# Optimization experiments

Measured on AMD Instinct MI355X. Metric: run time of the kernel, lower is better.

The kernel has to match this reference:

```python
import jax, jax.numpy as jnp
import numpy as np

B, T, A, K, STEPS, E = 2, 16384, 128, 128, 16, 126


def soft_dirac_last(x):
    # softmax forward-replaced by one-hot(argmax), straight-through backward
    sm = jax.nn.softmax(x, axis=-1)
    hard = jax.nn.one_hot(jnp.argmax(x, axis=-1), x.shape[-1], dtype=x.dtype)
    return sm + jax.lax.stop_gradient(hard - sm)


def _encode(x, d_unit, atom_embeddings):
    # x: (B,1,T); d_unit: (A,K) unit-norm atoms
    rng = jnp.linspace(0.0, 1.0, T, dtype=x.dtype)
    kernel = d_unit[:, None, :]  # OIH
    pad = [(K // 2, K - 1 - K // 2)]  # SAME
    batch_ix = jnp.arange(B)

    def step(res, _):
        # dense feature map: correlation of residual with every atom
        fm = jax.lax.conv_general_dilated(
            res, kernel, window_strides=(1,), padding=pad,
            dimension_numbers=("NCH", "OIH", "NCH"))  # (B,A,T)
        flat = fm.reshape(B, A * T)
        fi = jnp.argmax(flat, axis=-1)                      # sparsify n_to_keep=1
        value = jnp.take_along_axis(flat, fi[:, None], axis=-1)  # (B,1)
        ai = fi // T
        ti = fi % T
        # position: soft_dirac over time of sparse fm summed over atoms
        pos_row = jnp.zeros((B, T), x.dtype).at[batch_ix, ti].set(value[:, 0])
        pd = soft_dirac_last(pos_row)
        position = jnp.sum(pd * rng[None, :], axis=-1, keepdims=True) * 20.0  # (B,1)
        # atom one-hot: soft_dirac over atom axis of sparse fm summed over time
        atom_row = jnp.zeros((B, A), x.dtype).at[batch_ix, ai].set(value[:, 0])
        ad = soft_dirac_last(atom_row)
        ae = ad @ atom_embeddings  # (B,E)
        emb = jnp.concatenate([position, value, ae], axis=-1)  # (B, 2+E)
        # matching-pursuit residual update: subtract value * atom at found shift
        recon = value * d_unit[ai]  # (B,K)
        buf = jnp.zeros((B, T + K), x.dtype)
        buf = jax.vmap(lambda bb, rr, tt: jax.lax.dynamic_update_slice(bb, rr, (tt,)))(buf, recon, ti)
        res = res - buf[:, None, K // 2:K // 2 + T]
        return res, emb

    res, embs = jax.lax.scan(step, x, None, length=STEPS)
    embs = jnp.transpose(embs, (1, 0, 2))  # (B, STEPS, 2+E)
    return embs, res


def _canonical_ordering(embs, proj):
    keys = embs @ proj  # (B, STEPS)
    order = jnp.argsort(keys, axis=-1)
    return jnp.take_along_axis(embs, order[:, :, None], axis=1)


def setup_inputs() -> dict:
    key = jax.random.key(0)
    ks = jax.random.split(key, 5)
    return {
        "a": jax.random.normal(ks[0], (B, 1, T), jnp.float32),
        "b": jax.random.normal(ks[1], (B, 1, T), jnp.float32),
        "d": jax.random.normal(ks[2], (A, K), jnp.float32),
        "atom_embeddings": jax.random.normal(ks[3], (A, E), jnp.float32) * 0.1,
        "ordering_proj": jax.random.normal(ks[4], (128,), jnp.float32),
    }


def reference(a, b, d, atom_embeddings, ordering_proj):
    d_unit = d / (jnp.linalg.norm(d, axis=-1, keepdims=True) + 1e-8)
    ae, a_res = _encode(a, d_unit, atom_embeddings)
    be, b_res = _encode(b, d_unit, atom_embeddings)
    ae = _canonical_ordering(ae, ordering_proj)
    be = _canonical_ordering(be, ordering_proj)
    a_norm = jnp.linalg.norm(a_res.reshape(-1, T), axis=-1)
    b_norm = jnp.linalg.norm(b_res.reshape(-1, T), axis=-1)
    return jnp.mean((ae - be) ** 2) + jnp.mean(jnp.abs(a_norm - b_norm))
```

## Files before the change

kernel.cpp:

```cpp
#include <hip/hip_runtime.h>
#include <math.h>

#define T_DIM 16384
#define A_DIM 128
#define K_DIM 128
#define N_STEPS 16
#define E_DIM 126
#define NSEQ 4

#define ATI 16
#define TT 256
#define NPT 512
#define NCB 32
#define HB 8192
#define RL_LEN 8319
#define RL_PAD 8608
#define SS_LEN 383
#define SS_PAD 404

#define PIDX(i) ((i) + ((i) >> 5))

__device__ inline unsigned long long pack_vi(float v, int fi) {
    unsigned int b = __float_as_uint(v);
    b = (b & 0x80000000u) ? ~b : (b | 0x80000000u);
    return ((unsigned long long)b << 32) | (unsigned int)(~fi);
}
__device__ inline void unpack_vi(unsigned long long p, float* v, int* fi) {
    unsigned int lo = (unsigned int)(p & 0xffffffffu);
    unsigned int b = (unsigned int)(p >> 32);
    unsigned int fb = (b & 0x80000000u) ? (b & 0x7fffffffu) : ~b;
    *v = __uint_as_float(fb);
    *fi = (int)(~lo);
}

__device__ inline unsigned long long u64max(unsigned long long a, unsigned long long b) {
    return a > b ? a : b;
}

__global__ __launch_bounds__(256) void k_prep(
    const float* __restrict__ d, const float* __restrict__ a,
    const float* __restrict__ b, float* __restrict__ du,
    float* __restrict__ res, int* __restrict__ cnt,
    unsigned long long* __restrict__ slots) {
    int blk = blockIdx.x, tid = threadIdx.x;
    if (blk < 128) {
        __shared__ float s[128];
        float v = 0.0f;
        if (tid < 128) { v = d[blk * K_DIM + tid]; s[tid] = v * v; }
        __syncthreads();
        for (int off = 64; off > 0; off >>= 1) {
            if (tid < off) s[tid] += s[tid + off];
            __syncthreads();
        }
        if (tid < 128) du[blk * K_DIM + tid] = v / (sqrtf(s[0]) + 1e-8f);
    } else if (blk < 384) {
        int i = (blk - 128) * 256 + tid;
        res[i] = (i < 2 * T_DIM) ? a[i] : b[i - 2 * T_DIM];
    } else {
        if (tid < NSEQ) cnt[tid] = 0;
        for (int i = tid; i < (N_STEPS - 1) * NSEQ * 16 + (N_STEPS - 1) * NSEQ;
             i += 256) slots[i] = 0ULL;
    }
}

__device__ inline unsigned long long tile_compute(
    const float* __restrict__ duP, const float* __restrict__ rsh,
    int L0, int a_lo, int t_lo, int tid, unsigned long long* red4) {

    float acc[4][4];
    #pragma unroll
    for (int i = 0; i < 4; i++)
        #pragma unroll
        for (int j = 0; j < 4; j++) acc[i][j] = 0.0f;

    float r[8];
    #pragma unroll
    for (int m = 0; m < 8; m++) r[m] = rsh[PIDX(L0 + m)];

    #pragma unroll 4
    for (int k = 0; k < K_DIM; k += 4) {
        float dA[4][4];
        #pragma unroll
        for (int i = 0; i < 4; i++)
            *(float4*)dA[i] = *(const float4*)(duP + i * K_DIM + k);
        #pragma unroll
        for (int dk = 0; dk < 4; dk++) {
            #pragma unroll
            for (int i = 0; i < 4; i++) {
                float s = dA[i][dk];
                #pragma unroll
                for (int j = 0; j < 4; j++)
                    acc[i][j] = fmaf(s, r[j + dk], acc[i][j]);
            }
        }
        r[0] = r[4]; r[1] = r[5]; r[2] = r[6]; r[3] = r[7];
        #pragma unroll
        for (int m = 0; m < 4; m++) r[4 + m] = rsh[PIDX(L0 + k + 8 + m)];
    }

    float bv = -INFINITY;
    int bi = 0x7fffffff;
    #pragma unroll
    for (int i = 0; i < 4; i++) {
        int a = a_lo + i;
        #pragma unroll
        for (int j = 0; j < 4; j++) {
            int fi = a * T_DIM + t_lo + j;
            float v = acc[i][j];
            if (v > bv || (v == bv && fi < bi)) { bv = v; bi = fi; }
        }
    }
    #pragma unroll
    for (int off = 32; off > 0; off >>= 1) {
        float v2 = __shfl_down(bv, off);
        int   i2 = __shfl_down(bi, off);
        if (v2 > bv || (v2 == bv && i2 < bi)) { bv = v2; bi = i2; }
    }
    if ((tid & 63) == 0) red4[tid >> 6] = pack_vi(bv, bi);
    __syncthreads();
    if (tid == 0) {
        unsigned long long m = red4[0];
        #pragma unroll
        for (int w = 1; w < 4; w++) if (red4[w] > m) m = red4[w];
        red4[0] = m;
    }
    __syncthreads();
    return red4[0];
}

__global__ __launch_bounds__(256) void k_step_full(
    float* __restrict__ res, const float* __restrict__ du,
    const float* __restrict__ ae, float* __restrict__ emb,
    unsigned long long* __restrict__ pmax, int* __restrict__ cnt,
    int* __restrict__ dirty0) {

    int seq = blockIdx.y;
    int blk = blockIdx.x;
    int a_base = (blk >> 6) * ATI;
    int t0 = (blk & 63) * TT;
    int tid = threadIdx.x;

    __shared__ float rsh[SS_PAD];
    __shared__ unsigned long long red4[4];
    __shared__ unsigned long long pm_sh[256];
    __shared__ int last_flag;

    const float* resS = res + seq * T_DIM;
    for (int i = tid; i < SS_LEN; i += 256) {
        int t = t0 - 64 + i;
        rsh[PIDX(i)] = (t >= 0 && t < T_DIM) ? resS[t] : 0.0f;
    }
    __syncthreads();

    int tg = tid & 63;
    int ag = __builtin_amdgcn_readfirstlane(tid >> 6);
    unsigned long long p = tile_compute(du + (a_base + ag * 4) * K_DIM, rsh,
                                        4 * tg, a_base + ag * 4, t0 + 4 * tg,
                                        tid, red4);
    if (tid == 0) {
        pmax[seq * NPT + blk] = p;
        __threadfence();
        last_flag = (atomicAdd(&cnt[seq], 1) == NPT - 1);
    }
    __syncthreads();
    if (!last_flag) return;

    __threadfence();
    {
        unsigned long long m0 = pmax[seq * NPT + tid];
        unsigned long long m1 = pmax[seq * NPT + 256 + tid];
        pm_sh[tid] = u64max(m0, m1);
    }
    __syncthreads();
    for (int off = 128; off > 0; off >>= 1) {
        if (tid < off) pm_sh[tid] = u64max(pm_sh[tid], pm_sh[tid + off]);
        __syncthreads();
    }
    float value; int fi;
    unpack_vi(pm_sh[0], &value, &fi);
    int ai = fi >> 14;
    int ti = fi & (T_DIM - 1);
    int pos_idx = value > 0.0f ? ti : 0;
    int atom_idx = value > 0.0f ? ai : 0;

    float* e = emb + (seq * N_STEPS + 0) * 128;
    if (tid == 0) {
        e[0] = ((float)pos_idx / (float)(T_DIM - 1)) * 20.0f;
        e[1] = value;
        int nlo = ti - (K_DIM - 1); if (nlo < 0) nlo = 0;
        int nhi = ti + K_DIM;       if (nhi > T_DIM) nhi = T_DIM;
        dirty0[seq * 2 + 0] = nlo;
        dirty0[seq * 2 + 1] = nhi;
    }
    if (tid >= 2 && tid < 2 + E_DIM) e[tid] = ae[atom_idx * E_DIM + tid - 2];
    if (tid >= 128) {
        int k = tid - 128;
        int t = ti + k - K_DIM / 2;
        if (t >= 0 && t < T_DIM) {
            float r = res[seq * T_DIM + t];
            res[seq * T_DIM + t] = __fsub_rn(r, __fmul_rn(value, du[ai * K_DIM + k]));
        }
    }
}

__global__ __launch_bounds__(256) void k_inc(
    float* __restrict__ res, const float* __restrict__ du,
    const float* __restrict__ ae, float* __restrict__ emb,
    const unsigned long long* __restrict__ pmax,
    unsigned long long* __restrict__ dslots,
    unsigned long long* __restrict__ wslots, const int* __restrict__ dirty0) {

    int seq = blockIdx.y;
    int blk = blockIdx.x;
    int tid = threadIdx.x;

    if (blk == NCB) {
        __shared__ unsigned long long table[NPT];
        __shared__ unsigned long long red4[4];
        __shared__ unsigned long long wsh;
        for (int i = tid; i < NPT; i += 256) table[i] = pmax[seq * NPT + i];
        int lo = dirty0[seq * 2 + 0];
        int hi = dirty0[seq * 2 + 1];
        __syncthreads();

        for (int step = 1; step < N_STEPS; step++) {
            int T0 = lo >> 8, T1 = T0 + 1;
            bool hasT1 = (T1 < 64) && (T1 * TT < hi);
            if (tid < 16) {
                int a = tid >> 1, w = tid & 1;
                if (w == 0 || hasT1) {
                    const unsigned long long* sp =
                        &dslots[((step - 1) * NSEQ + seq) * 16 + tid];
                    unsigned long long v = __hip_atomic_load(sp, __ATOMIC_RELAXED,
                                                             __HIP_MEMORY_SCOPE_AGENT);
                    while (v == 0ULL) {
                        __builtin_amdgcn_s_sleep(1);
                        v = __hip_atomic_load(sp, __ATOMIC_RELAXED,
                                              __HIP_MEMORY_SCOPE_AGENT);
                    }
                    table[a * 64 + (w ? T1 : T0)] = v;
                }
            }
            __syncthreads();
            unsigned long long m = u64max(table[tid], table[tid + 256]);
            #pragma unroll
            for (int off = 32; off > 0; off >>= 1)
                m = u64max(m, __shfl_down(m, off));
            if ((tid & 63) == 0) red4[tid >> 6] = m;
            __syncthreads();
            if (tid == 0) {
                unsigned long long w = red4[0];
                #pragma unroll
                for (int j = 1; j < 4; j++) w = u64max(w, red4[j]);
                wsh = w;
                atomicExch(&wslots[(step - 1) * NSEQ + seq], w);
            }
            __syncthreads();
            float value; int fi;
            unpack_vi(wsh, &value, &fi);
            int ti = fi & (T_DIM - 1);
            int ai = fi >> 14;
            int pos_idx = value > 0.0f ? ti : 0;
            int atom_idx = value > 0.0f ? ai : 0;
            float* e = emb + (seq * N_STEPS + step) * 128;
            if (tid == 0) {
                e[0] = ((float)pos_idx / (float)(T_DIM - 1)) * 20.0f;
                e[1] = value;
            }
            if (tid >= 2 && tid < 128) e[tid] = ae[atom_idx * E_DIM + tid - 2];
            lo = ti - (K_DIM - 1); if (lo < 0) lo = 0;
            hi = ti + K_DIM;       if (hi > T_DIM) hi = T_DIM;
        }
        return;
    }

    int atile = blk >> 2;
    int half = (blk >> 1) & 1;
    int par = blk & 1;
    int a_base = atile * ATI;
    int base = half * HB;

    __shared__ float resL[RL_PAD];
    __shared__ unsigned long long red4[4];
    __shared__ unsigned long long wsh;

    const float* resG = res + seq * T_DIM;
    for (int i4 = tid * 4; i4 < RL_LEN; i4 += 1024) {
        int t = base - 64 + i4;
        if (t >= 0 && t + 3 < T_DIM && i4 + 3 < RL_LEN) {
            float4 v = *(const float4*)&resG[t];
            resL[PIDX(i4 + 0)] = v.x; resL[PIDX(i4 + 1)] = v.y;
            resL[PIDX(i4 + 2)] = v.z; resL[PIDX(i4 + 3)] = v.w;
        } else {
            for (int m = 0; m < 4 && i4 + m < RL_LEN; m++) {
                int t2 = t + m;
                resL[PIDX(i4 + m)] = (t2 >= 0 && t2 < T_DIM) ? resG[t2] : 0.0f;
            }
        }
    }
    int lo = dirty0[seq * 2 + 0];
    int hi = dirty0[seq * 2 + 1];
    __syncthreads();

    for (int step = 1; step < N_STEPS; step++) {
        int T0 = lo >> 8, T1 = T0 + 1;
        int cand = -1;
        if (((T0 & 1) == par) && ((T0 >> 5) == half)) cand = T0;
        else if (T1 < 64 && ((T1 & 1) == par) && ((T1 >> 5) == half) &&
                 T1 * TT < hi) cand = T1;

        if (cand >= 0) {
            int t0 = cand * TT;
            int tg = tid & 63;
            int ag = __builtin_amdgcn_readfirstlane(tid >> 6);
            unsigned long long p = tile_compute(
                du + (a_base + ag * 4) * K_DIM, resL,
                (t0 - base) + 4 * tg, a_base + ag * 4, t0 + 4 * tg, tid, red4);
            if (tid == 0)
                atomicExch(&dslots[((step - 1) * NSEQ + seq) * 16 +
                                   atile * 2 + (cand == T1 ? 1 : 0)], p);
        }
        if (tid == 0) {
            const unsigned long long* sp = &wslots[(step - 1) * NSEQ + seq];
            unsigned long long v = __hip_atomic_load(sp, __ATOMIC_RELAXED,
                                                     __HIP_MEMORY_SCOPE_AGENT);
            while (v == 0ULL) {
                __builtin_amdgcn_s_sleep(2);
                v = __hip_atomic_load(sp, __ATOMIC_RELAXED,
                                      __HIP_MEMORY_SCOPE_AGENT);
            }
            wsh = v;
        }
        __syncthreads();
        float value; int fi;
        unpack_vi(wsh, &value, &fi);
        int ti = fi & (T_DIM - 1);
        int ai = fi >> 14;
        if (tid < 128) {
            int t = ti - K_DIM / 2 + tid;
            if (t >= 0 && t < T_DIM) {
                int L = t - base + 64;
                if (L >= 0 && L < RL_LEN) {
                    float r = resL[PIDX(L)];
                    resL[PIDX(L)] = __fsub_rn(r, __fmul_rn(value, du[ai * K_DIM + tid]));
                }
            }
        }
        __syncthreads();
        lo = ti - (K_DIM - 1); if (lo < 0) lo = 0;
        hi = ti + K_DIM;       if (hi > T_DIM) hi = T_DIM;
    }

    if (atile == 0 && par == 0) {
        float* resW = res + seq * T_DIM + base;
        for (int t = tid; t < HB; t += 256) resW[t] = resL[PIDX(t + 64)];
    }
}

__global__ __launch_bounds__(1024) void k_tail(
    const float* __restrict__ res, const float* __restrict__ emb,
    const float* __restrict__ proj, float* __restrict__ out) {
    int tid = threadIdx.x;
    __shared__ float sh[1024];
    __shared__ float norms[NSEQ];
    __shared__ float keys[NSEQ][N_STEPS];
    __shared__ int   order[NSEQ][N_STEPS];

    {
        int seq = tid >> 8;
        int ln  = tid & 255;
        const float4* r4 = (const float4*)(res + seq * T_DIM);
        float s = 0.0f;
        #pragma unroll
        for (int j = 0; j < 16; j++) {
            float4 v = r4[j * 256 + ln];
            s = fmaf(v.x, v.x, s); s = fmaf(v.y, v.y, s);
            s = fmaf(v.z, v.z, s); s = fmaf(v.w, v.w, s);
        }
        sh[tid] = s;
        __syncthreads();
        for (int off = 128; off > 0; off >>= 1) {
            if (ln < off) sh[tid] += sh[tid + off];
            __syncthreads();
        }
        if (ln == 0) norms[seq] = sqrtf(sh[tid]);
        __syncthreads();
    }
    {
        int pair = tid >> 4;
        int seq = pair >> 4, st = pair & 15;
        int ln = tid & 15;
        const float* e = emb + (seq * N_STEPS + st) * 128 + ln * 8;
        const float* pr = proj + ln * 8;
        float kk = 0.0f;
        #pragma unroll
        for (int dd = 0; dd < 8; dd++) kk = fmaf(e[dd], pr[dd], kk);
        sh[tid] = kk;
        __syncthreads();
        for (int off = 8; off > 0; off >>= 1) {
            if (ln < off) sh[tid] += sh[tid + off];
            __syncthreads();
        }
        if (ln == 0) keys[seq][st] = sh[tid];
        __syncthreads();
    }
    if (tid < NSEQ) {
        int ord[N_STEPS];
        for (int i = 0; i < N_STEPS; i++) ord[i] = i;
        for (int i = 1; i < N_STEPS; i++) {
            int oi = ord[i];
            float kv = keys[tid][oi];
            int j = i - 1;
            while (j >= 0 && keys[tid][ord[j]] > kv) { ord[j + 1] = ord[j]; j--; }
            ord[j + 1] = oi;
        }
        for (int i = 0; i < N_STEPS; i++) order[tid][i] = ord[i];
    }
    __syncthreads();
    float s = 0.0f;
    #pragma unroll
    for (int t = 0; t < 4; t++) {
        int idx = tid + t * 1024;
        int b  = idx >> 11;
        int st = (idx >> 7) & 15;
        int dd = idx & 127;
        float va = emb[((b    ) * N_STEPS + order[b    ][st]) * 128 + dd];
        float vb = emb[((2 + b) * N_STEPS + order[2 + b][st]) * 128 + dd];
        float df = va - vb;
        s = fmaf(df, df, s);
    }
    sh[tid] = s;
    __syncthreads();
    for (int off = 512; off > 0; off >>= 1) {
        if (tid < off) sh[tid] += sh[tid + off];
        __syncthreads();
    }
    if (tid == 0) {
        float mse = sh[0] / 4096.0f;
        float mad = 0.5f * (fabsf(norms[0] - norms[2]) + fabsf(norms[1] - norms[3]));
        out[0] = mse + mad;
    }
}

extern "C" void kernel_launch(void* const* d_in, const int* in_sizes, int n_in,
                              void* d_out, int out_size, void* d_ws, size_t ws_size,
                              hipStream_t stream) {
    const float* a    = (const float*)d_in[0];
    const float* b    = (const float*)d_in[1];
    const float* d    = (const float*)d_in[2];
    const float* ae   = (const float*)d_in[3];
    const float* proj = (const float*)d_in[4];
    float* out = (float*)d_out;

    float* ws  = (float*)d_ws;
    float* res = ws;
    float* du  = res + NSEQ * T_DIM;
    float* emb = du + A_DIM * K_DIM;
    unsigned long long* pmax   = (unsigned long long*)(emb + NSEQ * N_STEPS * 128);
    unsigned long long* dslots = pmax + NSEQ * NPT;
    unsigned long long* wslots = dslots + (N_STEPS - 1) * NSEQ * 16;
    int* cnt    = (int*)(wslots + (N_STEPS - 1) * NSEQ);
    int* dirty0 = cnt + NSEQ;

    k_prep<<<385, 256, 0, stream>>>(d, a, b, du, res, cnt, dslots);

    dim3 gfull(NPT, NSEQ);
    k_step_full<<<gfull, 256, 0, stream>>>(res, du, ae, emb, pmax, cnt, dirty0);

    dim3 ginc(NCB + 1, NSEQ);
    k_inc<<<ginc, 256, 0, stream>>>(res, du, ae, emb, pmax, dslots, wslots, dirty0);

    k_tail<<<1, 1024, 0, stream>>>(res, emb, proj, out);
}
```

Baseline: 235.1 us.

## Drop global residual buffer, halve atom tile, fold norm into incremental kernel

The separate residual copy is removed: the full-step and incremental kernels read the inputs a/b directly, and the first matching-pursuit subtraction is applied on the fly while loading into shared memory. The atom tile is halved from 16 to 8 atoms per block, which doubles the number of tiles in the full pass and in the incremental pass. That gives more parallelism, but each tile does less reuse. Residual norms are now accumulated with an atomic add at the end of k_inc instead of writing the residual back and re-reading it in k_tail. This removes global traffic but changes the float summation order.

```diff
diff --git a/kernel.cpp b/kernel.cpp
--- a/kernel.cpp
+++ b/kernel.cpp
@@ -8,10 +8,12 @@
 #define E_DIM 126
 #define NSEQ 4
 
-#define ATI 16
+#define ATI 8
+#define NAT 16
 #define TT 256
-#define NPT 512
-#define NCB 32
+#define NTT 64
+#define NPT 1024
+#define NCB 64
 #define HB 8192
 #define RL_LEN 8319
 #define RL_PAD 8608
@@ -32,16 +34,14 @@
     *v = __uint_as_float(fb);
     *fi = (int)(~lo);
 }
-
 __device__ inline unsigned long long u64max(unsigned long long a, unsigned long long b) {
     return a > b ? a : b;
 }
 
 __global__ __launch_bounds__(256) void k_prep(
-    const float* __restrict__ d, const float* __restrict__ a,
-    const float* __restrict__ b, float* __restrict__ du,
-    float* __restrict__ res, int* __restrict__ cnt,
-    unsigned long long* __restrict__ slots) {
+    const float* __restrict__ d, float* __restrict__ du,
+    unsigned long long* __restrict__ zeroU, int* __restrict__ cnt,
+    float* __restrict__ norm2) {
     int blk = blockIdx.x, tid = threadIdx.x;
     if (blk < 128) {
         __shared__ float s[128];
@@ -53,13 +53,9 @@
             __syncthreads();
         }
         if (tid < 128) du[blk * K_DIM + tid] = v / (sqrtf(s[0]) + 1e-8f);
-    } else if (blk < 384) {
-        int i = (blk - 128) * 256 + tid;
-        res[i] = (i < 2 * T_DIM) ? a[i] : b[i - 2 * T_DIM];
     } else {
-        if (tid < NSEQ) cnt[tid] = 0;
-        for (int i = tid; i < (N_STEPS - 1) * NSEQ * 16 + (N_STEPS - 1) * NSEQ;
-             i += 256) slots[i] = 0ULL;
+        for (int i = tid; i < 1984; i += 256) zeroU[i] = 0ULL;
+        if (tid < NSEQ) { cnt[tid] = 0; norm2[tid] = 0.0f; }
     }
 }
 
@@ -67,9 +63,9 @@
     const float* __restrict__ duP, const float* __restrict__ rsh,
     int L0, int a_lo, int t_lo, int tid, unsigned long long* red4) {
 
-    float acc[4][4];
+    float acc[2][4];
     #pragma unroll
-    for (int i = 0; i < 4; i++)
+    for (int i = 0; i < 2; i++)
         #pragma unroll
         for (int j = 0; j < 4; j++) acc[i][j] = 0.0f;
 
@@ -79,14 +75,14 @@
 
     #pragma unroll 4
     for (int k = 0; k < K_DIM; k += 4) {
-        float dA[4][4];
-        #pragma unroll
-        for (int i = 0; i < 4; i++)
+        float dA[2][4];
+        #pragma unroll
+        for (int i = 0; i < 2; i++)
             *(float4*)dA[i] = *(const float4*)(duP + i * K_DIM + k);
         #pragma unroll
         for (int dk = 0; dk < 4; dk++) {
             #pragma unroll
-            for (int i = 0; i < 4; i++) {
+            for (int i = 0; i < 2; i++) {
                 float s = dA[i][dk];
                 #pragma unroll
                 for (int j = 0; j < 4; j++)
@@ -101,7 +97,7 @@
     float bv = -INFINITY;
     int bi = 0x7fffffff;
     #pragma unroll
-    for (int i = 0; i < 4; i++) {
+    for (int i = 0; i < 2; i++) {
         int a = a_lo + i;
         #pragma unroll
         for (int j = 0; j < 4; j++) {
@@ -121,7 +117,7 @@
     if (tid == 0) {
         unsigned long long m = red4[0];
         #pragma unroll
-        for (int w = 1; w < 4; w++) if (red4[w] > m) m = red4[w];
+        for (int w = 1; w < 4; w++) m = u64max(m, red4[w]);
         red4[0] = m;
     }
     __syncthreads();
@@ -129,10 +125,11 @@
 }
 
 __global__ __launch_bounds__(256) void k_step_full(
-    float* __restrict__ res, const float* __restrict__ du,
-    const float* __restrict__ ae, float* __restrict__ emb,
-    unsigned long long* __restrict__ pmax, int* __restrict__ cnt,
-    int* __restrict__ dirty0) {
+    const float* __restrict__ a, const float* __restrict__ b,
+    const float* __restrict__ du, const float* __restrict__ ae,
+    float* __restrict__ emb, unsigned long long* __restrict__ pmax,
+    int* __restrict__ cnt, int* __restrict__ dirty0,
+    unsigned long long* __restrict__ w0slot) {
 
     int seq = blockIdx.y;
     int blk = blockIdx.x;
@@ -145,17 +142,17 @@
     __shared__ unsigned long long pm_sh[256];
     __shared__ int last_flag;
 
-    const float* resS = res + seq * T_DIM;
+    const float* x = (seq < 2 ? a : b) + (seq & 1) * T_DIM;
     for (int i = tid; i < SS_LEN; i += 256) {
         int t = t0 - 64 + i;
-        rsh[PIDX(i)] = (t >= 0 && t < T_DIM) ? resS[t] : 0.0f;
+        rsh[PIDX(i)] = (t >= 0 && t < T_DIM) ? x[t] : 0.0f;
     }
     __syncthreads();
 
     int tg = tid & 63;
     int ag = __builtin_amdgcn_readfirstlane(tid >> 6);
-    unsigned long long p = tile_compute(du + (a_base + ag * 4) * K_DIM, rsh,
-                                        4 * tg, a_base + ag * 4, t0 + 4 * tg,
+    unsigned long long p = tile_compute(du + (a_base + ag * 2) * K_DIM, rsh,
+                                        4 * tg, a_base + ag * 2, t0 + 4 * tg,
                                         tid, red4);
     if (tid == 0) {
         pmax[seq * NPT + blk] = p;
@@ -167,9 +164,11 @@
 
     __threadfence();
     {
-        unsigned long long m0 = pmax[seq * NPT + tid];
-        unsigned long long m1 = pmax[seq * NPT + 256 + tid];
-        pm_sh[tid] = u64max(m0, m1);
+        unsigned long long m = u64max(pmax[seq * NPT + tid],
+                                      pmax[seq * NPT + 256 + tid]);
+        m = u64max(m, u64max(pmax[seq * NPT + 512 + tid],
+                             pmax[seq * NPT + 768 + tid]));
+        pm_sh[tid] = m;
     }
     __syncthreads();
     for (int off = 128; off > 0; off >>= 1) {
@@ -191,24 +190,19 @@
         int nhi = ti + K_DIM;       if (nhi > T_DIM) nhi = T_DIM;
         dirty0[seq * 2 + 0] = nlo;
         dirty0[seq * 2 + 1] = nhi;
+        w0slot[seq] = pm_sh[0];
     }
     if (tid >= 2 && tid < 2 + E_DIM) e[tid] = ae[atom_idx * E_DIM + tid - 2];
-    if (tid >= 128) {
-        int k = tid - 128;
-        int t = ti + k - K_DIM / 2;
-        if (t >= 0 && t < T_DIM) {
-            float r = res[seq * T_DIM + t];
-            res[seq * T_DIM + t] = __fsub_rn(r, __fmul_rn(value, du[ai * K_DIM + k]));
-        }
-    }
 }
 
 __global__ __launch_bounds__(256) void k_inc(
-    float* __restrict__ res, const float* __restrict__ du,
-    const float* __restrict__ ae, float* __restrict__ emb,
-    const unsigned long long* __restrict__ pmax,
+    const float* __restrict__ a, const float* __restrict__ b,
+    const float* __restrict__ du, const float* __restrict__ ae,
+    float* __restrict__ emb, const unsigned long long* __restrict__ pmax,
     unsigned long long* __restrict__ dslots,
-    unsigned long long* __restrict__ wslots, const int* __restrict__ dirty0) {
+    unsigned long long* __restrict__ wslot,
+    const unsigned long long* __restrict__ w0slot,
+    const int* __restrict__ dirty0, float* __restrict__ norm2) {
 
     int seq = blockIdx.y;
     int blk = blockIdx.x;
@@ -217,7 +211,6 @@
     if (blk == NCB) {
         __shared__ unsigned long long table[NPT];
         __shared__ unsigned long long red4[4];
-        __shared__ unsigned long long wsh;
         for (int i = tid; i < NPT; i += 256) table[i] = pmax[seq * NPT + i];
         int lo = dirty0[seq * 2 + 0];
         int hi = dirty0[seq * 2 + 1];
@@ -225,12 +218,12 @@
 
         for (int step = 1; step < N_STEPS; step++) {
             int T0 = lo >> 8, T1 = T0 + 1;
-            bool hasT1 = (T1 < 64) && (T1 * TT < hi);
-            if (tid < 16) {
-                int a = tid >> 1, w = tid & 1;
+            bool hasT1 = (T1 < NTT) && (T1 * TT < hi);
+            if (tid < 2 * NAT) {
+                int at = tid >> 1, w = tid & 1;
                 if (w == 0 || hasT1) {
                     const unsigned long long* sp =
-                        &dslots[((step - 1) * NSEQ + seq) * 16 + tid];
+                        &dslots[((step - 1) * NSEQ + seq) * (2 * NAT) + tid];
                     unsigned long long v = __hip_atomic_load(sp, __ATOMIC_RELAXED,
                                                              __HIP_MEMORY_SCOPE_AGENT);
                     while (v == 0ULL) {
@@ -238,26 +231,29 @@
                         v = __hip_atomic_load(sp, __ATOMIC_RELAXED,
                                               __HIP_MEMORY_SCOPE_AGENT);
                     }
-                    table[a * 64 + (w ? T1 : T0)] = v;
+                    table[at * NTT + (w ? T1 : T0)] = v;
                 }
             }
             __syncthreads();
             unsigned long long m = u64max(table[tid], table[tid + 256]);
+            m = u64max(m, u64max(table[tid + 512], table[tid + 768]));
             #pragma unroll
             for (int off = 32; off > 0; off >>= 1)
                 m = u64max(m, __shfl_down(m, off));
             if ((tid & 63) == 0) red4[tid >> 6] = m;
             __syncthreads();
+            unsigned long long w;
             if (tid == 0) {
-                unsigned long long w = red4[0];
+                w = red4[0];
                 #pragma unroll
                 for (int j = 1; j < 4; j++) w = u64max(w, red4[j]);
-                wsh = w;
-                atomicExch(&wslots[(step - 1) * NSEQ + seq], w);
-            }
-            __syncthreads();
+                red4[0] = w;
+                atomicExch(&wslot[(step - 1) * NSEQ + seq], w);
+            }
+            __syncthreads();
+            w = red4[0];
             float value; int fi;
-            unpack_vi(wsh, &value, &fi);
+            unpack_vi(w, &value, &fi);
             int ti = fi & (T_DIM - 1);
             int ai = fi >> 14;
             int pos_idx = value > 0.0f ? ti : 0;
@@ -283,20 +279,28 @@
     __shared__ float resL[RL_PAD];
     __shared__ unsigned long long red4[4];
     __shared__ unsigned long long wsh;
-
-    const float* resG = res + seq * T_DIM;
-    for (int i4 = tid * 4; i4 < RL_LEN; i4 += 1024) {
-        int t = base - 64 + i4;
-        if (t >= 0 && t + 3 < T_DIM && i4 + 3 < RL_LEN) {
-            float4 v = *(const float4*)&resG[t];
-            resL[PIDX(i4 + 0)] = v.x; resL[PIDX(i4 + 1)] = v.y;
-            resL[PIDX(i4 + 2)] = v.z; resL[PIDX(i4 + 3)] = v.w;
-        } else {
-            for (int m = 0; m < 4 && i4 + m < RL_LEN; m++) {
-                int t2 = t + m;
-                resL[PIDX(i4 + m)] = (t2 >= 0 && t2 < T_DIM) ? resG[t2] : 0.0f;
-            }
-        }
+    __shared__ float w0v_s; __shared__ int w0t_s, w0a_s;
+    __shared__ float snorm[256];
+
+    if (tid == 0) {
+        float v; int fi;
+        unpack_vi(w0slot[seq], &v, &fi);
+        w0v_s = v; w0t_s = fi & (T_DIM - 1); w0a_s = fi >> 14;
+    }
+    __syncthreads();
+    float w0v = w0v_s; int w0t = w0t_s, w0a = w0a_s;
+
+    const float* x = (seq < 2 ? a : b) + (seq & 1) * T_DIM;
+    for (int i = tid; i < RL_LEN; i += 256) {
+        int t = base - 64 + i;
+        float v = 0.0f;
+        if (t >= 0 && t < T_DIM) {
+            v = x[t];
+            int dk = t - (w0t - K_DIM / 2);
+            if (dk >= 0 && dk < K_DIM)
+                v = __fsub_rn(v, __fmul_rn(w0v, du[w0a * K_DIM + dk]));
+        }
+        resL[PIDX(i)] = v;
     }
     int lo = dirty0[seq * 2 + 0];
     int hi = dirty0[seq * 2 + 1];
@@ -306,7 +310,7 @@
         int T0 = lo >> 8, T1 = T0 + 1;
         int cand = -1;
         if (((T0 & 1) == par) && ((T0 >> 5) == half)) cand = T0;
-        else if (T1 < 64 && ((T1 & 1) == par) && ((T1 >> 5) == half) &&
+        else if (T1 < NTT && ((T1 & 1) == par) && ((T1 >> 5) == half) &&
                  T1 * TT < hi) cand = T1;
 
         if (cand >= 0) {
@@ -314,14 +318,14 @@
             int tg = tid & 63;
             int ag = __builtin_amdgcn_readfirstlane(tid >> 6);
             unsigned long long p = tile_compute(
-                du + (a_base + ag * 4) * K_DIM, resL,
-                (t0 - base) + 4 * tg, a_base + ag * 4, t0 + 4 * tg, tid, red4);
+                du + (a_base + ag * 2) * K_DIM, resL,
+                (t0 - base) + 4 * tg, a_base + ag * 2, t0 + 4 * tg, tid, red4);
             if (tid == 0)
-                atomicExch(&dslots[((step - 1) * NSEQ + seq) * 16 +
+                atomicExch(&dslots[((step - 1) * NSEQ + seq) * (2 * NAT) +
                                    atile * 2 + (cand == T1 ? 1 : 0)], p);
         }
         if (tid == 0) {
-            const unsigned long long* sp = &wslots[(step - 1) * NSEQ + seq];
+            const unsigned long long* sp = &wslot[(step - 1) * NSEQ + seq];
             unsigned long long v = __hip_atomic_load(sp, __ATOMIC_RELAXED,
                                                      __HIP_MEMORY_SCOPE_AGENT);
             while (v == 0ULL) {
@@ -332,6 +336,7 @@
             wsh = v;
         }
         __syncthreads();
+
         float value; int fi;
         unpack_vi(wsh, &value, &fi);
         int ti = fi & (T_DIM - 1);
@@ -352,40 +357,31 @@
     }
 
     if (atile == 0 && par == 0) {
-        float* resW = res + seq * T_DIM + base;
-        for (int t = tid; t < HB; t += 256) resW[t] = resL[PIDX(t + 64)];
+        float s = 0.0f;
+        for (int t = tid; t < HB; t += 256) {
+            float v = resL[PIDX(t + 64)];
+            s = fmaf(v, v, s);
+        }
+        snorm[tid] = s;
+        __syncthreads();
+        for (int off = 128; off > 0; off >>= 1) {
+            if (tid < off) snorm[tid] += snorm[tid + off];
+            __syncthreads();
+        }
+        if (tid == 0) atomicAdd(&norm2[seq], snorm[0]);
     }
 }
 
 __global__ __launch_bounds__(1024) void k_tail(
-    const float* __restrict__ res, const float* __restrict__ emb,
-    const float* __restrict__ proj, float* __restrict__ out) {
+    const float* __restrict__ emb, const float* __restrict__ proj,
+    const float* __restrict__ norm2, float* __restrict__ out) {
     int tid = threadIdx.x;
     __shared__ float sh[1024];
     __shared__ float norms[NSEQ];
     __shared__ float keys[NSEQ][N_STEPS];
     __shared__ int   order[NSEQ][N_STEPS];
 
-    {
-        int seq = tid >> 8;
-        int ln  = tid & 255;
-        const float4* r4 = (const float4*)(res + seq * T_DIM);
-        float s = 0.0f;
-        #pragma unroll
-        for (int j = 0; j < 16; j++) {
-            float4 v = r4[j * 256 + ln];
-            s = fmaf(v.x, v.x, s); s = fmaf(v.y, v.y, s);
-            s = fmaf(v.z, v.z, s); s = fmaf(v.w, v.w, s);
-        }
-        sh[tid] = s;
-        __syncthreads();
-        for (int off = 128; off > 0; off >>= 1) {
-            if (ln < off) sh[tid] += sh[tid + off];
-            __syncthreads();
-        }
-        if (ln == 0) norms[seq] = sqrtf(sh[tid]);
-        __syncthreads();
-    }
+    if (tid < NSEQ) norms[tid] = sqrtf(norm2[tid]);
     {
         int pair = tid >> 4;
         int seq = pair >> 4, st = pair & 15;
@@ -421,11 +417,11 @@
     #pragma unroll
     for (int t = 0; t < 4; t++) {
         int idx = tid + t * 1024;
-        int b  = idx >> 11;
+        int bq = idx >> 11;
         int st = (idx >> 7) & 15;
         int dd = idx & 127;
-        float va = emb[((b    ) * N_STEPS + order[b    ][st]) * 128 + dd];
-        float vb = emb[((2 + b) * N_STEPS + order[2 + b][st]) * 128 + dd];
+        float va = emb[((bq    ) * N_STEPS + order[bq    ][st]) * 128 + dd];
+        float vb = emb[((2 + bq) * N_STEPS + order[2 + bq][st]) * 128 + dd];
         float df = va - vb;
         s = fmaf(df, df, s);
     }
@@ -453,22 +449,25 @@
     float* out = (float*)d_out;
 
     float* ws  = (float*)d_ws;
-    float* res = ws;
-    float* du  = res + NSEQ * T_DIM;
+    float* du  = ws;
     float* emb = du + A_DIM * K_DIM;
     unsigned long long* pmax   = (unsigned long long*)(emb + NSEQ * N_STEPS * 128);
     unsigned long long* dslots = pmax + NSEQ * NPT;
-    unsigned long long* wslots = dslots + (N_STEPS - 1) * NSEQ * 16;
-    int* cnt    = (int*)(wslots + (N_STEPS - 1) * NSEQ);
+    unsigned long long* wslot  = dslots + (N_STEPS - 1) * NSEQ * 2 * NAT;
+    unsigned long long* w0slot = wslot + (N_STEPS - 1) * NSEQ;
+    int* cnt    = (int*)(w0slot + NSEQ);
     int* dirty0 = cnt + NSEQ;
-
-    k_prep<<<385, 256, 0, stream>>>(d, a, b, du, res, cnt, dslots);
+    float* norm2 = (float*)(dirty0 + 2 * NSEQ);
+
+    k_prep<<<129, 256, 0, stream>>>(d, du, dslots, cnt, norm2);
 
     dim3 gfull(NPT, NSEQ);
-    k_step_full<<<gfull, 256, 0, stream>>>(res, du, ae, emb, pmax, cnt, dirty0);
+    k_step_full<<<gfull, 256, 0, stream>>>(a, b, du, ae, emb, pmax, cnt,
+                                           dirty0, w0slot);
 
     dim3 ginc(NCB + 1, NSEQ);
-    k_inc<<<ginc, 256, 0, stream>>>(res, du, ae, emb, pmax, dslots, wslots, dirty0);
-
-    k_tail<<<1, 1024, 0, stream>>>(res, emb, proj, out);
-}
+    k_inc<<<ginc, 256, 0, stream>>>(a, b, du, ae, emb, pmax, dslots, wslot,
+                                    w0slot, dirty0, norm2);
+
+    k_tail<<<1, 1024, 0, stream>>>(emb, proj, norm2, out);
+}
```

After: 248.2 us. 5.6% more time.
